# Optimization experiments

Measured on AMD Instinct MI355X. Metric: run time of the kernel, lower is better.

Reference implementation:

```python
import jax, jax.numpy as jnp
import numpy as np

B, S, D, H, N, E = 4, 2048, 512, 8, 1024, 16384


def setup_inputs() -> dict:
    key = jax.random.key(0)
    ks = jax.random.split(key, 16)
    rn = lambda k, shp, s=0.02: jax.random.normal(k, shp, jnp.float32) * s
    x = jax.random.normal(ks[0], (B, S, D), jnp.float32)
    edge_index = jax.random.randint(ks[1], (2, E), 0, N)
    # unique sorted node positions per batch (equivalent to node_mask with N ones)
    node_indices = jnp.sort(
        jax.vmap(lambda k: jax.random.permutation(k, S)[:N])(jax.random.split(ks[2], B)),
        axis=1,
    )
    z = lambda shp: jnp.zeros(shp, jnp.float32)
    o = lambda shp: jnp.ones(shp, jnp.float32)
    return {
        "x": x,
        "edge_index": edge_index,
        "node_indices": node_indices,
        "Wq": rn(ks[3], (D, D)), "bq": z((D,)),
        "Wk": rn(ks[4], (D, D)), "bk": z((D,)),
        "Wv": rn(ks[5], (D, D)), "bv": z((D,)),
        "Wo": rn(ks[6], (D, D)), "bo": z((D,)),
        "Wf1": rn(ks[7], (D, 4 * D)), "bf1": z((4 * D,)),
        "Wf2": rn(ks[8], (4 * D, D)), "bf2": z((D,)),
        "g1": o((D,)), "be1": z((D,)),
        "g2": o((D,)), "be2": z((D,)),
        "g3": o((D,)), "be3": z((D,)),
        "Wg": rn(ks[9], (2 * D, D)), "bg": z((D,)),
        "Wgs": rn(ks[10], (D, D)), "Wgn": rn(ks[11], (D, D)), "bgn": z((D,)),
    }


def _ln(t, g, b, eps=1e-5):
    m = t.mean(-1, keepdims=True)
    v = ((t - m) ** 2).mean(-1, keepdims=True)
    return (t - m) * jax.lax.rsqrt(v + eps) * g + b


def reference(x, edge_index, node_indices, Wq, bq, Wk, bk, Wv, bv, Wo, bo,
              Wf1, bf1, Wf2, bf2, g1, be1, g2, be2, g3, be3, Wg, bg,
              Wgs, Wgn, bgn):
    Bs, Ss, Ds = x.shape
    Hn = H
    hd = Ds // Hn
    Nn = node_indices.shape[1]

    # --- self-attention (pre-norm, residual; dropout = eval identity) ---
    nx = _ln(x, g1, be1)
    q = (nx @ Wq + bq).reshape(Bs, Ss, Hn, hd).transpose(0, 2, 1, 3)
    k = (nx @ Wk + bk).reshape(Bs, Ss, Hn, hd).transpose(0, 2, 1, 3)
    v = (nx @ Wv + bv).reshape(Bs, Ss, Hn, hd).transpose(0, 2, 1, 3)
    scores = jnp.einsum('bhqd,bhkd->bhqk', q, k) / jnp.sqrt(jnp.float32(hd))
    attn = jax.nn.softmax(scores, axis=-1)
    ao = jnp.einsum('bhqk,bhkd->bhqd', attn, v).transpose(0, 2, 1, 3).reshape(Bs, Ss, Ds)
    x = x + ao @ Wo + bo

    # --- gather -> GNN -> scatter with sigmoid gate fusion ---
    nx2 = _ln(x, g2, be2)
    bidx = jnp.arange(Bs)[:, None]
    nodes = nx2[bidx, node_indices]                       # [B, N, D] gather
    src, dst = edge_index[0], edge_index[1]
    msgs = nodes[:, src, :]                               # [B, E, D]
    agg = jax.vmap(lambda m: jax.ops.segment_sum(m, dst, num_segments=Nn))(msgs)
    upd = jax.nn.relu(nodes @ Wgs + agg @ Wgn + bgn)      # GCN-like update
    gnn_out = jnp.zeros_like(nx2).at[bidx, node_indices].set(upd)  # scatter-back
    gate = jax.nn.sigmoid(jnp.concatenate([nx2, gnn_out], axis=-1) @ Wg + bg)
    x = x + gate * gnn_out + (1.0 - gate) * nx2

    # --- feed-forward ---
    nx3 = _ln(x, g3, be3)
    x = x + jax.nn.gelu(nx3 @ Wf1 + bf1, approximate=False) @ Wf2 + bf2
    return x
```

## Files before the change

kernel.cpp:

```cpp
#include <hip/hip_runtime.h>
#include <math.h>

using u16 = unsigned short;
using u32 = unsigned int;

typedef __attribute__((ext_vector_type(8))) short bf16x8;
typedef __attribute__((ext_vector_type(4))) float f32x4;

#define B_   4
#define S_   2048
#define D_   512
#define H_   8
#define HD_  64
#define N_   1024
#define E_   16384
#define DFF_ 2048
#define BS_  (B_ * S_)
#define BN_  (B_ * N_)
#define QSCALE 0.18033688011112042f
#define KSPLIT 2

__device__ __forceinline__ float bf2f(u16 u) {
  u32 v = (u32)u << 16; float f; __builtin_memcpy(&f, &v, 4); return f;
}
__device__ __forceinline__ u16 f2bf(float f) {
  u32 u; __builtin_memcpy(&u, &f, 4);
  u = u + 0x7fffu + ((u >> 16) & 1u);
  return (u16)(u >> 16);
}
__device__ __forceinline__ float bflo(u32 w) {
  u32 v = w << 16; float f; __builtin_memcpy(&f, &v, 4); return f;
}
__device__ __forceinline__ float bfhi(u32 w) {
  u32 v = w & 0xffff0000u; float f; __builtin_memcpy(&f, &v, 4); return f;
}
__device__ __forceinline__ u32 fbits(float f) { u32 u; __builtin_memcpy(&u, &f, 4); return u; }

__global__ __launch_bounds__(256) void tpose_all(const float* __restrict__ Wq, const float* __restrict__ Wk,
                                                 const float* __restrict__ Wv, const float* __restrict__ Wo,
                                                 const float* __restrict__ Wgs, const float* __restrict__ Wgn,
                                                 const float* __restrict__ Wg, const float* __restrict__ Wf1,
                                                 const float* __restrict__ Wf2, u16* __restrict__ wsbase) {
  __shared__ u16 t[32][33];
  const int z = blockIdx.z;
  const float* src; int C, r0, c0, ds, co; long doff;
  const long SL = 262144;
  switch (z) {
    case 0:  src = Wq;  C = 512;  r0 = 0;   c0 = 0;    ds = 512;  co = 0;   doff = 0;       break;
    case 1:  src = Wk;  C = 512;  r0 = 0;   c0 = 0;    ds = 512;  co = 0;   doff = 1 * SL;  break;
    case 2:  src = Wv;  C = 512;  r0 = 0;   c0 = 0;    ds = 512;  co = 0;   doff = 2 * SL;  break;
    case 3:  src = Wo;  C = 512;  r0 = 0;   c0 = 0;    ds = 512;  co = 0;   doff = 3 * SL;  break;
    case 4:  src = Wg;  C = 512;  r0 = 0;   c0 = 0;    ds = 1024; co = 0;   doff = 4 * SL;  break;
    case 5:  src = Wg;  C = 512;  r0 = 512; c0 = 0;    ds = 1024; co = 512; doff = 4 * SL;  break;
    case 6:  src = Wgs; C = 512;  r0 = 0;   c0 = 0;    ds = 1024; co = 0;   doff = 6 * SL;  break;
    case 7:  src = Wgn; C = 512;  r0 = 0;   c0 = 0;    ds = 1024; co = 512; doff = 6 * SL;  break;
    case 8: case 9: case 10: case 11:
             src = Wf1; C = 2048; r0 = 0;   c0 = (z - 8) * 512;  ds = 512;  co = 0; doff = 8 * SL;  break;
    default: src = Wf2; C = 512;  r0 = (z - 12) * 512; c0 = 0;   ds = 2048; co = (z - 12) * 512; doff = 12 * SL; break;
  }
  u16* dst = wsbase + doff;
  int rb = blockIdx.x * 32, cb = blockIdx.y * 32 + c0;
  int tx = threadIdx.x, ty = threadIdx.y;
  #pragma unroll
  for (int i = ty; i < 32; i += 8) t[i][tx] = f2bf(src[(long)(r0 + rb + i) * C + cb + tx]);
  __syncthreads();
  #pragma unroll
  for (int i = ty; i < 32; i += 8) dst[(long)(cb + i) * ds + co + rb + tx] = t[tx][i];
}

__global__ void packb_k(const float* __restrict__ bq, const float* __restrict__ bk,
                        const float* __restrict__ bv, float* __restrict__ o) {
  int i = blockIdx.x * 256 + threadIdx.x;
  if (i < 512) o[i] = bq[i];
  else if (i < 1024) o[i] = bk[i - 512];
  else if (i < 1536) o[i] = bv[i - 1024];
}

__global__ __launch_bounds__(256) void ln_k(const float* __restrict__ x, const float* __restrict__ g,
                                            const float* __restrict__ be, u16* __restrict__ out) {
  __shared__ float red[8];
  long row = blockIdx.x;
  int t = threadIdx.x;
  const float* xr = x + row * D_;
  float2 v = *(const float2*)(xr + 2 * t);
  float s = v.x + v.y, sq = v.x * v.x + v.y * v.y;
  #pragma unroll
  for (int m = 32; m >= 1; m >>= 1) { s += __shfl_xor(s, m, 64); sq += __shfl_xor(sq, m, 64); }
  if ((t & 63) == 0) { red[t >> 6] = s; red[4 + (t >> 6)] = sq; }
  __syncthreads();
  s = red[0] + red[1] + red[2] + red[3];
  sq = red[4] + red[5] + red[6] + red[7];
  float mean = s * (1.f / D_);
  float var = sq * (1.f / D_) - mean * mean;
  float rs = rsqrtf(fmaxf(var, 0.f) + 1e-5f);
  float2 gw = *(const float2*)(g + 2 * t);
  float2 bw = *(const float2*)(be + 2 * t);
  u32 o = (u32)f2bf((v.x - mean) * rs * gw.x + bw.x) | ((u32)f2bf((v.y - mean) * rs * gw.y + bw.y) << 16);
  *(u32*)&out[row * D_ + 2 * t] = o;
}

__device__ __forceinline__ void async_cp16(const u16* g, u16* l) {
  __builtin_amdgcn_global_load_lds((const __attribute__((address_space(1))) void*)g,
                                   (__attribute__((address_space(3))) void*)l, 16, 0, 0);
}

enum { EPI_QKV3, EPI_XF32, EPI_BF, EPI_RELU_SCATTER, EPI_GELU };

template <int EPI, bool CAT = false, int TM = 128>
__global__ __launch_bounds__(256) void gemm_k(const u16* __restrict__ A, const u16* __restrict__ A2,
                                              const u16* __restrict__ Bt, const float* __restrict__ bias,
                                              const void* src, void* out, const int* __restrict__ rowmap,
                                              int M, int N, int K) {
  constexpr int MT = TM / 32;
  __shared__ __align__(16) u16 As[2 * TM * 32];
  __shared__ __align__(16) u16 Bs[8192];
  int tid = threadIdx.x;
  int lane = tid & 63;
  int wn = (tid >> 6) & 1;
  int wm = (tid >> 7) & 1;
  long m0 = (long)blockIdx.y * TM;
  long n0 = (long)blockIdx.x * 128;

  f32x4 acc[MT][4];
  {
    f32x4 z = {0.f, 0.f, 0.f, 0.f};
    #pragma unroll
    for (int i = 0; i < MT; i++)
      #pragma unroll
      for (int j = 0; j < 4; j++) acc[i][j] = z;
  }

  int srow = tid >> 2;
  int skoff = (tid & 3) * 8;
  const int astride = CAT ? 512 : K;
  const u16* Ag  = A + (m0 + srow) * (long)astride + skoff;
  const u16* A2g = CAT ? (A2 + (m0 + srow) * (long)astride + skoff) : nullptr;
  const u16* Bg  = Bt + (n0 + srow) * (long)K + skoff;
  int rsel = lane & 15;
  int kchunk = (lane >> 4) * 8;

  for (int kt = 0; kt < K; kt += 64) {
    __syncthreads();
    #pragma unroll
    for (int s = 0; s < 2; s++) {
      int kts = kt + s * 32;
      const u16* Asrc = (CAT && kts >= 512) ? (A2g + (kts - 512)) : (Ag + kts);
      async_cp16(Asrc, As + s * (TM * 32) + tid * 8);
      if constexpr (TM == 128) async_cp16(Asrc + (long)64 * astride, As + s * (TM * 32) + 2048 + tid * 8);
      async_cp16(Bg + kts, Bs + s * 4096 + tid * 8);
      async_cp16(Bg + (long)64 * K + kts, Bs + s * 4096 + 2048 + tid * 8);
    }
    __syncthreads();
    #pragma unroll
    for (int s = 0; s < 2; s++) {
      bf16x8 af[MT], bfv[4];
      #pragma unroll
      for (int mt = 0; mt < MT; mt++)
        af[mt] = *(const bf16x8*)&As[s * (TM * 32) + (wm * (TM / 2) + mt * 16 + rsel) * 32 + kchunk];
      #pragma unroll
      for (int nt = 0; nt < 4; nt++)
        bfv[nt] = *(const bf16x8*)&Bs[s * 4096 + (wn * 64 + nt * 16 + rsel) * 32 + kchunk];
      #pragma unroll
      for (int mt = 0; mt < MT; mt++)
        #pragma unroll
        for (int nt = 0; nt < 4; nt++)
          acc[mt][nt] = __builtin_amdgcn_mfma_f32_16x16x32_bf16(af[mt], bfv[nt], acc[mt][nt], 0, 0, 0);
    }
  }

  int rbase = (lane >> 4) * 4;
  int cbase = lane & 15;
  #pragma unroll
  for (int mt = 0; mt < MT; mt++) {
    #pragma unroll
    for (int nt = 0; nt < 4; nt++) {
      long col = n0 + wn * 64 + nt * 16 + cbase;
      float bv = bias ? bias[col] : 0.f;
      long row0 = m0 + wm * (TM / 2) + mt * 16 + rbase;
      float vals[4];
      #pragma unroll
      for (int r = 0; r < 4; r++) vals[r] = acc[mt][nt][r] + bv;
      if constexpr (EPI == EPI_QKV3) {
        long which = col >> 9;
        long cc = col & 511;
        long b = row0 >> 11;
        long h = cc >> 6, d = cc & 63;
        if (which == 2) {
          long sI0 = row0 & 2047;
          uint2 w;
          w.x = (u32)f2bf(vals[0]) | ((u32)f2bf(vals[1]) << 16);
          w.y = (u32)f2bf(vals[2]) | ((u32)f2bf(vals[3]) << 16);
          *(uint2*)&((u16*)out)[2 * (long)BS_ * D_ + (((b * H_ + h) * HD_) + d) * S_ + sI0] = w;
        } else {
          #pragma unroll
          for (int r = 0; r < 4; r++) {
            long sI = (row0 + r) & 2047;
            float v2 = (which == 0) ? vals[r] * QSCALE : vals[r];
            ((u16*)out)[which * (long)BS_ * D_ + (((b * H_ + h) * S_) + sI) * HD_ + d] = f2bf(v2);
          }
        }
      } else {
        #pragma unroll
        for (int r = 0; r < 4; r++) {
          long row = row0 + r;
          float val = vals[r];
          if constexpr (EPI == EPI_XF32) {
            ((float*)out)[row * N + col] = val + ((const float*)src)[row * N + col];
          } else if constexpr (EPI == EPI_BF) {
            ((u16*)out)[row * N + col] = f2bf(val);
          } else if constexpr (EPI == EPI_RELU_SCATTER) {
            long orow = rowmap[row];
            ((u16*)out)[orow * D_ + col] = f2bf(fmaxf(val, 0.f));
          } else if constexpr (EPI == EPI_GELU) {
            ((u16*)out)[row * N + col] = f2bf(0.5f * val * (1.f + erff(val * 0.70710678118654752f)));
          }
        }
      }
    }
  }
}

__global__ __launch_bounds__(256) void attn_k(const u16* __restrict__ Q, const u16* __restrict__ Kv,
                                              const u16* __restrict__ VT, u16* __restrict__ Opart,
                                              float* __restrict__ Lp) {
  int tid = threadIdx.x;
  int lane = tid & 63;
  int wave = tid >> 6;
  int col = lane & 15;
  int quad = lane >> 4;
  int bh = blockIdx.y;
  int q0 = blockIdx.x * 128;
  int khalf = blockIdx.z;
  long base = (long)bh * S_;
  long vbase = (long)bh * HD_ * S_;

  const u16* qpa = Q + (base + q0 + wave * 32 + col) * HD_;
  const u16* qpb = qpa + 16 * HD_;
  bf16x8 bqa0 = *(const bf16x8*)(qpa + quad * 8);
  bf16x8 bqa1 = *(const bf16x8*)(qpa + 32 + quad * 8);
  bf16x8 bqb0 = *(const bf16x8*)(qpb + quad * 8);
  bf16x8 bqb1 = *(const bf16x8*)(qpb + 32 + quad * 8);

  float la = 0.f, lb = 0.f;
  f32x4 accA[4], accB[4];
  {
    f32x4 z = {0.f, 0.f, 0.f, 0.f};
    #pragma unroll
    for (int mt = 0; mt < 4; mt++) { accA[mt] = z; accB[mt] = z; }
  }

  const bool hiQ = (quad >= 2);
  const int s0 = (quad & 1) * 2;
  const int a0 = (s0 * 16 + col + wave * 64) * 4;
  const int a1 = ((s0 + 1) * 16 + col + wave * 64) * 4;

  const u16* kfb = Kv + (base + col) * HD_ + quad * 8;
  const u16* vfb = VT + vbase + (long)col * S_ + quad * 8;

  int kt0 = khalf * (S_ / KSPLIT);
  for (int kt = kt0; kt < kt0 + S_ / KSPLIT; kt += 64) {
    f32x4 sa[4], sb[4];
    #pragma unroll
    for (int nt = 0; nt < 4; nt++) {
      const u16* kp = kfb + (long)(kt + nt * 16) * HD_;
      bf16x8 ak0 = *(const bf16x8*)kp;
      bf16x8 ak1 = *(const bf16x8*)(kp + 32);
      f32x4 z = {0.f, 0.f, 0.f, 0.f};
      z = __builtin_amdgcn_mfma_f32_16x16x32_bf16(ak0, bqa0, z, 0, 0, 0);
      z = __builtin_amdgcn_mfma_f32_16x16x32_bf16(ak1, bqa1, z, 0, 0, 0);
      sa[nt] = z;
      f32x4 y = {0.f, 0.f, 0.f, 0.f};
      y = __builtin_amdgcn_mfma_f32_16x16x32_bf16(ak0, bqb0, y, 0, 0, 0);
      y = __builtin_amdgcn_mfma_f32_16x16x32_bf16(ak1, bqb1, y, 0, 0, 0);
      sb[nt] = y;
    }

    u32 pka[4][2], pkb[4][2];
    #pragma unroll
    for (int nt = 0; nt < 4; nt++) {
      #pragma unroll
      for (int r = 0; r < 4; r++) { sa[nt][r] = __builtin_amdgcn_exp2f(sa[nt][r]); sb[nt][r] = __builtin_amdgcn_exp2f(sb[nt][r]); }
      la += (sa[nt][0] + sa[nt][1]) + (sa[nt][2] + sa[nt][3]);
      lb += (sb[nt][0] + sb[nt][1]) + (sb[nt][2] + sb[nt][3]);
      pka[nt][0] = __builtin_amdgcn_perm(fbits(sa[nt][1]), fbits(sa[nt][0]), 0x07060302u);
      pka[nt][1] = __builtin_amdgcn_perm(fbits(sa[nt][3]), fbits(sa[nt][2]), 0x07060302u);
      pkb[nt][0] = __builtin_amdgcn_perm(fbits(sb[nt][1]), fbits(sb[nt][0]), 0x07060302u);
      pkb[nt][1] = __builtin_amdgcn_perm(fbits(sb[nt][3]), fbits(sb[nt][2]), 0x07060302u);
    }

    union { u32 d[4]; bf16x8 v; } ba0, ba1, bb0, bb1;
    {
      u32 sA = hiQ ? pka[1][0] : pka[0][0];
      u32 sB = hiQ ? pka[1][1] : pka[0][1];
      ba0.d[0] = __builtin_amdgcn_ds_bpermute(a0, sA);
      ba0.d[1] = __builtin_amdgcn_ds_bpermute(a0, sB);
      ba0.d[2] = __builtin_amdgcn_ds_bpermute(a1, sA);
      ba0.d[3] = __builtin_amdgcn_ds_bpermute(a1, sB);
      u32 sC = hiQ ? pka[3][0] : pka[2][0];
      u32 sD = hiQ ? pka[3][1] : pka[2][1];
      ba1.d[0] = __builtin_amdgcn_ds_bpermute(a0, sC);
      ba1.d[1] = __builtin_amdgcn_ds_bpermute(a0, sD);
      ba1.d[2] = __builtin_amdgcn_ds_bpermute(a1, sC);
      ba1.d[3] = __builtin_amdgcn_ds_bpermute(a1, sD);
      u32 tA = hiQ ? pkb[1][0] : pkb[0][0];
      u32 tB = hiQ ? pkb[1][1] : pkb[0][1];
      bb0.d[0] = __builtin_amdgcn_ds_bpermute(a0, tA);
      bb0.d[1] = __builtin_amdgcn_ds_bpermute(a0, tB);
      bb0.d[2] = __builtin_amdgcn_ds_bpermute(a1, tA);
      bb0.d[3] = __builtin_amdgcn_ds_bpermute(a1, tB);
      u32 tC = hiQ ? pkb[3][0] : pkb[2][0];
      u32 tD = hiQ ? pkb[3][1] : pkb[2][1];
      bb1.d[0] = __builtin_amdgcn_ds_bpermute(a0, tC);
      bb1.d[1] = __builtin_amdgcn_ds_bpermute(a0, tD);
      bb1.d[2] = __builtin_amdgcn_ds_bpermute(a1, tC);
      bb1.d[3] = __builtin_amdgcn_ds_bpermute(a1, tD);
    }

    #pragma unroll
    for (int mt = 0; mt < 4; mt++) {
      const u16* vp = vfb + (long)(mt * 16) * S_ + kt;
      bf16x8 av0 = *(const bf16x8*)vp;
      bf16x8 av1 = *(const bf16x8*)(vp + 32);
      accA[mt] = __builtin_amdgcn_mfma_f32_16x16x32_bf16(av0, ba0.v, accA[mt], 0, 0, 0);
      accA[mt] = __builtin_amdgcn_mfma_f32_16x16x32_bf16(av1, ba1.v, accA[mt], 0, 0, 0);
      accB[mt] = __builtin_amdgcn_mfma_f32_16x16x32_bf16(av0, bb0.v, accB[mt], 0, 0, 0);
      accB[mt] = __builtin_amdgcn_mfma_f32_16x16x32_bf16(av1, bb1.v, accB[mt], 0, 0, 0);
    }
  }

  la += __shfl_xor(la, 16, 64);
  la += __shfl_xor(la, 32, 64);
  lb += __shfl_xor(lb, 16, 64);
  lb += __shfl_xor(lb, 32, 64);

  int b = bh >> 3, h = bh & 7;
  long qrowA = (long)(b * S_) + q0 + wave * 32 + col;
  u16* Pp = Opart + (long)khalf * BS_ * D_;
  if (quad == 0) {
    float* lr = Lp + ((long)(khalf * 32 + bh)) * S_ + q0 + wave * 32;
    lr[col] = la;
    lr[16 + col] = lb;
  }
  u16* opA = Pp + qrowA * D_ + h * HD_ + quad * 4;
  u16* opB = Pp + (qrowA + 16) * D_ + h * HD_ + quad * 4;
  #pragma unroll
  for (int mt = 0; mt < 4; mt++) {
    uint2 w;
    w.x = (u32)f2bf(accA[mt][0]) | ((u32)f2bf(accA[mt][1]) << 16);
    w.y = (u32)f2bf(accA[mt][2]) | ((u32)f2bf(accA[mt][3]) << 16);
    *(uint2*)(opA + mt * 16) = w;
    uint2 v;
    v.x = (u32)f2bf(accB[mt][0]) | ((u32)f2bf(accB[mt][1]) << 16);
    v.y = (u32)f2bf(accB[mt][2]) | ((u32)f2bf(accB[mt][3]) << 16);
    *(uint2*)(opB + mt * 16) = v;
  }
}

__global__ __launch_bounds__(256) void acomb_k(const u16* __restrict__ P, const float* __restrict__ Lp,
                                               u16* __restrict__ AO) {
  long i = (long)blockIdx.x * 256 + threadIdx.x;
  long e0 = i * 4;
  long tok = e0 >> 9;
  int hh = (int)((e0 >> 6) & 7);
  long s = tok & 2047;
  long bb = tok >> 11;
  long bh = bb * 8 + hh;
  float l = 0.f;
  float v0 = 0.f, v1 = 0.f, v2 = 0.f, v3 = 0.f;
  #pragma unroll
  for (int k = 0; k < KSPLIT; k++) {
    uint2 a = ((const uint2*)(P + (long)k * BS_ * D_))[i];
    v0 += bflo(a.x); v1 += bfhi(a.x);
    v2 += bflo(a.y); v3 += bfhi(a.y);
    l += Lp[((long)(k * 32) + bh) * S_ + s];
  }
  float inv = 1.f / l;
  uint2 o;
  o.x = (u32)f2bf(v0 * inv) | ((u32)f2bf(v1 * inv) << 16);
  o.y = (u32)f2bf(v2 * inv) | ((u32)f2bf(v3 * inv) << 16);
  ((uint2*)AO)[i] = o;
}

__global__ __launch_bounds__(128) void gather_k(const u16* __restrict__ nx2, const int* __restrict__ nidx,
                                                int* __restrict__ rowmap, u16* __restrict__ Acat) {
  int bn = blockIdx.x;
  int t = threadIdx.x;
  long srow = (long)(bn >> 10) * S_ + nidx[bn];
  if (t == 0) rowmap[bn] = (int)srow;
  const u32* sp = (const u32*)(nx2 + srow * D_);
  u32* dp = (u32*)(Acat + (long)bn * 1024);
  dp[t] = sp[t];
  dp[t + 128] = sp[t + 128];
}

#define DEG_CAP 256
__global__ __launch_bounds__(256) void agg_k(const int* __restrict__ ei, u16* __restrict__ Acat) {
  __shared__ int cnt;
  __shared__ int lst[DEG_CAP];
  int n = blockIdx.x;
  int t = threadIdx.x;
  if (t == 0) cnt = 0;
  __syncthreads();
  const int* dst = ei + E_;
  for (int e = t; e < E_; e += 256) {
    if (dst[e] == n) {
      int idx = atomicAdd(&cnt, 1);
      if (idx < DEG_CAP) lst[idx] = ei[e];
    }
  }
  __syncthreads();
  int mcnt = cnt < DEG_CAP ? cnt : DEG_CAP;
  float2 acc[4] = {{0.f, 0.f}, {0.f, 0.f}, {0.f, 0.f}, {0.f, 0.f}};
  for (int i = 0; i < mcnt; i++) {
    long s = lst[i];
    #pragma unroll
    for (int b = 0; b < 4; b++) {
      u32 w = *(const u32*)&Acat[((long)(b * N_) + s) * 1024 + 2 * t];
      acc[b].x += bflo(w);
      acc[b].y += bfhi(w);
    }
  }
  #pragma unroll
  for (int b = 0; b < 4; b++) {
    u32 r = (u32)f2bf(acc[b].x) | ((u32)f2bf(acc[b].y) << 16);
    *(u32*)&Acat[((long)(b * N_) + n) * 1024 + 512 + 2 * t] = r;
  }
}

__global__ __launch_bounds__(256) void combln_k(const float* __restrict__ x1, const u16* __restrict__ gpre,
                                                const u16* __restrict__ gnn, const u16* __restrict__ nx2,
                                                const float* __restrict__ g3, const float* __restrict__ be3,
                                                float* __restrict__ x2, u16* __restrict__ nx3) {
  __shared__ float red[8];
  long row = blockIdx.x;
  int t = threadIdx.x;
  long off = row * D_ + 2 * t;
  float2 a = *(const float2*)(x1 + off);
  u32 gp = *(const u32*)(gpre + off);
  u32 gn = *(const u32*)(gnn + off);
  u32 nv = *(const u32*)(nx2 + off);
  float g0 = 1.f / (1.f + __expf(-bflo(gp)));
  float g1 = 1.f / (1.f + __expf(-bfhi(gp)));
  float t0 = a.x + g0 * bflo(gn) + (1.f - g0) * bflo(nv);
  float t1 = a.y + g1 * bfhi(gn) + (1.f - g1) * bfhi(nv);
  float2 w = {t0, t1};
  *(float2*)(x2 + off) = w;
  float s = t0 + t1, sq = t0 * t0 + t1 * t1;
  #pragma unroll
  for (int m = 32; m >= 1; m >>= 1) { s += __shfl_xor(s, m, 64); sq += __shfl_xor(sq, m, 64); }
  if ((t & 63) == 0) { red[t >> 6] = s; red[4 + (t >> 6)] = sq; }
  __syncthreads();
  s = red[0] + red[1] + red[2] + red[3];
  sq = red[4] + red[5] + red[6] + red[7];
  float mean = s * (1.f / D_);
  float var = sq * (1.f / D_) - mean * mean;
  float rs = rsqrtf(fmaxf(var, 0.f) + 1e-5f);
  float2 gw = *(const float2*)(g3 + 2 * t);
  float2 bw = *(const float2*)(be3 + 2 * t);
  u32 o = (u32)f2bf((t0 - mean) * rs * gw.x + bw.x) | ((u32)f2bf((t1 - mean) * rs * gw.y + bw.y) << 16);
  *(u32*)&nx3[off] = o;
}

extern "C" void kernel_launch(void* const* d_in, const int* in_sizes, int n_in,
                              void* d_out, int out_size, void* d_ws, size_t ws_size,
                              hipStream_t stream) {
  const float* x  = (const float*)d_in[0];
  const int* ei   = (const int*)d_in[1];
  const int* nidx = (const int*)d_in[2];
  const float* Wq = (const float*)d_in[3];   const float* bq = (const float*)d_in[4];
  const float* Wk = (const float*)d_in[5];   const float* bk = (const float*)d_in[6];
  const float* Wv = (const float*)d_in[7];   const float* bv = (const float*)d_in[8];
  const float* Wo = (const float*)d_in[9];   const float* bo = (const float*)d_in[10];
  const float* Wf1 = (const float*)d_in[11]; const float* bf1 = (const float*)d_in[12];
  const float* Wf2 = (const float*)d_in[13]; const float* bf2v = (const float*)d_in[14];
  const float* g1 = (const float*)d_in[15];  const float* be1 = (const float*)d_in[16];
  const float* g2 = (const float*)d_in[17];  const float* be2 = (const float*)d_in[18];
  const float* g3 = (const float*)d_in[19];  const float* be3 = (const float*)d_in[20];
  const float* Wg = (const float*)d_in[21];  const float* bg = (const float*)d_in[22];
  const float* Wgs = (const float*)d_in[23]; const float* Wgn = (const float*)d_in[24];
  const float* bgn = (const float*)d_in[25];

  const size_t MB8 = (size_t)8 * 1024 * 1024;
  char* base = (char*)d_ws;
  const size_t SLOT = (size_t)512 * 512 * 2;
  u16* WqT     = (u16*)(base + 0 * SLOT);
  u16* WoT     = (u16*)(base + 3 * SLOT);
  u16* WgFullT = (u16*)(base + 4 * SLOT);
  u16* WgsgnT  = (u16*)(base + 6 * SLOT);
  u16* Wf1T    = (u16*)(base + 8 * SLOT);
  u16* Wf2T    = (u16*)(base + 12 * SLOT);

  char* RA   = base + 16 * SLOT;
  char* Rqb  = RA + MB8;
  char* Rkb  = Rqb + MB8;
  char* Rvb  = Rkb + MB8;
  char* Rac  = Rvb + MB8;
  char* Rag  = Rac + MB8;
  char* Rx2  = Rag + MB8;
  char* RM   = Rx2 + 2 * MB8;

  u16* nx   = (u16*)RA;   u16* ao  = (u16*)RA;   u16* gnn = (u16*)RA;  u16* nx3 = (u16*)RA;
  u16* qb   = (u16*)Rqb;
  float* x1 = (float*)Rqb;
  u16* nx2  = (u16*)Rvb;
  u16* Opart = (u16*)Rac;
  u16* Acat = (u16*)Rac;
  u16* gpre = (u16*)Rac;
  float* x2 = (float*)Rx2;
  u16* ffh  = (u16*)Rqb;
  int* rowmap = (int*)RM;
  float* qkvb = (float*)(RM + 16384);
  float* Lpart = (float*)(RM + 32768);

  dim3 tb(32, 8);
  tpose_all<<<dim3(16, 16, 16), tb, 0, stream>>>(Wq, Wk, Wv, Wo, Wgs, Wgn, Wg, Wf1, Wf2, (u16*)base);
  packb_k<<<6, 256, 0, stream>>>(bq, bk, bv, qkvb);

  ln_k<<<BS_, 256, 0, stream>>>(x, g1, be1, nx);
  gemm_k<EPI_QKV3, false, 128><<<dim3(12, 64), 256, 0, stream>>>(nx, nullptr, WqT, qkvb, nullptr, qb, nullptr, BS_, 1536, 512);
  attn_k<<<dim3(S_ / 128, B_ * H_, KSPLIT), 256, 0, stream>>>(qb, qb + (long)BS_ * D_, qb + 2 * (long)BS_ * D_, Opart, Lpart);
  acomb_k<<<(BS_ * D_) / (256 * 4), 256, 0, stream>>>(Opart, Lpart, ao);
  gemm_k<EPI_XF32, false, 64><<<dim3(4, 128), 256, 0, stream>>>(ao, nullptr, WoT, bo, x, x1, nullptr, BS_, 512, 512);

  ln_k<<<BS_, 256, 0, stream>>>(x1, g2, be2, nx2);
  gather_k<<<BN_, 128, 0, stream>>>(nx2, nidx, rowmap, Acat);
  hipMemsetAsync(gnn, 0, (size_t)BS_ * D_ * 2, stream);
  agg_k<<<N_, 256, 0, stream>>>(ei, Acat);
  gemm_k<EPI_RELU_SCATTER, false, 64><<<dim3(4, 64), 256, 0, stream>>>(Acat, nullptr, WgsgnT, bgn, nullptr, gnn, rowmap, BN_, 512, 1024);

  gemm_k<EPI_BF, true, 64><<<dim3(4, 128), 256, 0, stream>>>(nx2, gnn, WgFullT, bg, nullptr, gpre, nullptr, BS_, 512, 1024);
  combln_k<<<BS_, 256, 0, stream>>>(x1, gpre, gnn, nx2, g3, be3, x2, nx3);

  gemm_k<EPI_GELU, false, 128><<<dim3(16, 64), 256, 0, stream>>>(nx3, nullptr, Wf1T, bf1, nullptr, ffh, nullptr, BS_, DFF_, 512);
  gemm_k<EPI_XF32, false, 64><<<dim3(4, 128), 256, 0, stream>>>(ffh, nullptr, Wf2T, bf2v, x2, (float*)d_out, nullptr, BS_, 512, DFF_);
}
```

Measured before the change: 485.4 us.

## Stage attention K/V tiles in padded LDS and swizzle GEMM block order

The attention kernel now loads each 64-key K and V^T tile cooperatively into padded shared memory, and all four waves read from it. Before, every wave fetched the same tiles from global memory itself. The GEMM kernel also remaps workgroup IDs in an XCD-aware interleave, so that neighbouring tiles land on the same die and L2 reuse improves. In exchange, attention gains two barriers per iteration with no double buffering, which exposes global load latency.

```diff
diff --git a/kernel.cpp b/kernel.cpp
--- a/kernel.cpp
+++ b/kernel.cpp
@@ -18,6 +18,7 @@
 #define BS_  (B_ * S_)
 #define BN_  (B_ * N_)
 #define QSCALE 0.18033688011112042f
+#define KSTRIDE 68
 #define KSPLIT 2
 
 __device__ __forceinline__ float bf2f(u16 u) {
@@ -118,8 +119,13 @@
   int lane = tid & 63;
   int wn = (tid >> 6) & 1;
   int wm = (tid >> 7) & 1;
-  long m0 = (long)blockIdx.y * TM;
-  long n0 = (long)blockIdx.x * 128;
+  int nwg = gridDim.x * gridDim.y;
+  int orig = blockIdx.y * gridDim.x + blockIdx.x;
+  int wgid = ((orig & 7) * (nwg >> 3)) + (orig >> 3);
+  int bx = wgid % gridDim.x;
+  int by = wgid / gridDim.x;
+  long m0 = (long)by * TM;
+  long n0 = (long)bx * 128;
 
   f32x4 acc[MT][4];
   {
@@ -223,6 +229,8 @@
 __global__ __launch_bounds__(256) void attn_k(const u16* __restrict__ Q, const u16* __restrict__ Kv,
                                               const u16* __restrict__ VT, u16* __restrict__ Opart,
                                               float* __restrict__ Lp) {
+  __shared__ __align__(16) u16 Ks[64 * KSTRIDE];
+  __shared__ __align__(16) u16 Vs[64 * KSTRIDE];
   int tid = threadIdx.x;
   int lane = tid & 63;
   int wave = tid >> 6;
@@ -249,22 +257,31 @@
     for (int mt = 0; mt < 4; mt++) { accA[mt] = z; accB[mt] = z; }
   }
 
+  int srow = tid >> 2;
+  int sdc = (tid & 3) * 16;
   const bool hiQ = (quad >= 2);
   const int s0 = (quad & 1) * 2;
   const int a0 = (s0 * 16 + col + wave * 64) * 4;
   const int a1 = ((s0 + 1) * 16 + col + wave * 64) * 4;
 
-  const u16* kfb = Kv + (base + col) * HD_ + quad * 8;
-  const u16* vfb = VT + vbase + (long)col * S_ + quad * 8;
-
   int kt0 = khalf * (S_ / KSPLIT);
   for (int kt = kt0; kt < kt0 + S_ / KSPLIT; kt += 64) {
+    __syncthreads();
+    {
+      const u16* kg = Kv + (base + kt + srow) * HD_ + sdc;
+      *(bf16x8*)&Ks[srow * KSTRIDE + sdc]     = *(const bf16x8*)kg;
+      *(bf16x8*)&Ks[srow * KSTRIDE + sdc + 8] = *(const bf16x8*)(kg + 8);
+      const u16* vg = VT + (vbase + (long)srow * S_) + kt + sdc;
+      *(bf16x8*)&Vs[srow * KSTRIDE + sdc]     = *(const bf16x8*)vg;
+      *(bf16x8*)&Vs[srow * KSTRIDE + sdc + 8] = *(const bf16x8*)(vg + 8);
+    }
+    __syncthreads();
+
     f32x4 sa[4], sb[4];
     #pragma unroll
     for (int nt = 0; nt < 4; nt++) {
-      const u16* kp = kfb + (long)(kt + nt * 16) * HD_;
-      bf16x8 ak0 = *(const bf16x8*)kp;
-      bf16x8 ak1 = *(const bf16x8*)(kp + 32);
+      bf16x8 ak0 = *(const bf16x8*)&Ks[(nt * 16 + col) * KSTRIDE + quad * 8];
+      bf16x8 ak1 = *(const bf16x8*)&Ks[(nt * 16 + col) * KSTRIDE + 32 + quad * 8];
       f32x4 z = {0.f, 0.f, 0.f, 0.f};
       z = __builtin_amdgcn_mfma_f32_16x16x32_bf16(ak0, bqa0, z, 0, 0, 0);
       z = __builtin_amdgcn_mfma_f32_16x16x32_bf16(ak1, bqa1, z, 0, 0, 0);
@@ -318,9 +335,8 @@
 
     #pragma unroll
     for (int mt = 0; mt < 4; mt++) {
-      const u16* vp = vfb + (long)(mt * 16) * S_ + kt;
-      bf16x8 av0 = *(const bf16x8*)vp;
-      bf16x8 av1 = *(const bf16x8*)(vp + 32);
+      bf16x8 av0 = *(const bf16x8*)&Vs[(mt * 16 + col) * KSTRIDE + quad * 8];
+      bf16x8 av1 = *(const bf16x8*)&Vs[(mt * 16 + col) * KSTRIDE + 32 + quad * 8];
       accA[mt] = __builtin_amdgcn_mfma_f32_16x16x32_bf16(av0, ba0.v, accA[mt], 0, 0, 0);
       accA[mt] = __builtin_amdgcn_mfma_f32_16x16x32_bf16(av1, ba1.v, accA[mt], 0, 0, 0);
       accB[mt] = __builtin_amdgcn_mfma_f32_16x16x32_bf16(av0, bb0.v, accB[mt], 0, 0, 0);
```

Measured after the change: 401.5 us. 1.21x faster.
